# Kernel tuning notes

Measured on AMD Instinct MI355X. Metric: run time of the kernel, lower is better.

## Reference

```python
import jax, jax.numpy as jnp
import numpy as np

# Config constants derived from init_kwargs
VX, VY = 0.16, 0.16
X0, Y0 = 0.0, -39.68
X_OFF = VX / 2 + X0
Y_OFF = VY / 2 + Y0
X_L, Y_L = 432, 496  # round((x1-x0)/vx), round((y1-y0)/vy)
B = 4
C_OUT = 64
BN_EPS = 1e-3


def setup_inputs() -> dict:
    key = jax.random.key(0)
    ks = jax.random.split(key, 9)
    M, P = 64000, 32
    pillars = jax.random.normal(ks[0], (M, P, 4), dtype=jnp.float32)
    b_id = jax.random.randint(ks[1], (M,), 0, B, dtype=jnp.int32)
    z_id = jnp.zeros((M,), dtype=jnp.int32)
    y_id = jax.random.randint(ks[2], (M,), 0, Y_L, dtype=jnp.int32)
    x_id = jax.random.randint(ks[3], (M,), 0, X_L, dtype=jnp.int32)
    coors = jnp.stack([b_id, z_id, y_id, x_id], axis=1)
    nums = jax.random.randint(ks[4], (M,), 1, P + 1, dtype=jnp.int32)
    W = jax.random.normal(ks[5], (C_OUT, 9), dtype=jnp.float32) * 0.1
    gamma = 1.0 + 0.1 * jax.random.normal(ks[6], (C_OUT,), dtype=jnp.float32)
    beta = 0.1 * jax.random.normal(ks[7], (C_OUT,), dtype=jnp.float32)
    running_mean = 0.1 * jax.random.normal(ks[8], (C_OUT,), dtype=jnp.float32)
    running_var = jax.random.uniform(ks[8], (C_OUT,), dtype=jnp.float32, minval=0.5, maxval=1.5)
    return {"pillars": pillars, "coors": coors, "nums": nums, "W": W,
            "gamma": gamma, "beta": beta,
            "running_mean": running_mean, "running_var": running_var}


def reference(pillars, coors, nums, W, gamma, beta, running_mean, running_var):
    M, P, _ = pillars.shape
    numsf = nums.astype(jnp.float32)
    point_mask = (jnp.arange(P)[None, :] < nums[:, None]).astype(pillars.dtype)  # [M,P]

    # mean of valid xyz per pillar, center features
    masked_xyz = pillars[:, :, :3] * point_mask[:, :, None]
    mean = masked_xyz.sum(axis=1, keepdims=True) / jnp.clip(numsf, 1.0)[:, None, None]
    f_centered = pillars[:, :, :3] - mean

    # offsets from pillar center
    x_c = coors[:, 3].astype(jnp.float32) * VX + X_OFF
    y_c = coors[:, 2].astype(jnp.float32) * VY + Y_OFF
    f_x = pillars[:, :, 0:1] - x_c[:, None, None]
    f_y = pillars[:, :, 1:2] - y_c[:, None, None]

    features = jnp.concatenate([pillars, f_centered, f_x, f_y], axis=2)  # [M,P,9]
    features = features * point_mask[:, :, None]

    # 1x1 conv + eval-mode BN + ReLU, then max over points
    h = jnp.einsum('mpc,oc->mpo', features, W)  # [M,P,C_OUT]
    scale = gamma / jnp.sqrt(running_var + BN_EPS)
    h = jax.nn.relu(h * scale + (beta - running_mean * scale))
    pooled = h.max(axis=1)  # [M,C_OUT]

    b = coors[:, 0]
    y = coors[:, 2]
    x = coors[:, 3]
    valid = (x >= 0) & (x < X_L) & (y >= 0) & (y < Y_L)
    y_s = jnp.where(valid, y, Y_L)
    x_s = jnp.where(valid, x, X_L)
    canvas = jnp.zeros((B, Y_L, X_L, C_OUT), dtype=pooled.dtype)
    canvas = canvas.at[b, y_s, x_s].set(pooled, mode='drop')
    return canvas.transpose(0, 3, 1, 2)  # [B, C_OUT, Y_L, X_L]
```

## Files before the change

kernel.cpp:

```cpp
#include <hip/hip_runtime.h>

#define XL 432
#define XL4 108
#define YL 496
#define CELLS_B (YL * XL)
#define PLANE4 (CELLS_B / 4)
#define BN 4
#define COUT 64
#define PP 32
#define TCELLS 128
#define TG 32
#define LSTR 132

__global__ __launch_bounds__(256) void winner_kernel(const int* __restrict__ coors,
                                                     int* __restrict__ winner, int M) {
    int m = blockIdx.x * blockDim.x + threadIdx.x;
    if (m >= M) return;
    int b = coors[4 * m + 0];
    int y = coors[4 * m + 2];
    int x = coors[4 * m + 3];
    if (x < 0 || x >= XL || y < 0 || y >= YL) return;
    atomicMax(&winner[(b * YL + y) * XL + x], m);
}

__global__ __launch_bounds__(256) void pillar_compute(
    const float* __restrict__ pillars,
    const int* __restrict__ coors,
    const int* __restrict__ nums,
    const float* __restrict__ W,
    const float* __restrict__ gamma, const float* __restrict__ beta,
    const float* __restrict__ rmean, const float* __restrict__ rvar,
    float* __restrict__ pooled,
    int M) {
    const int pb   = threadIdx.x >> 6;
    const int lane = threadIdx.x & 63;
    const int m    = blockIdx.x * 4 + pb;

    __shared__ float4 pts[4][PP];

    if (m < M && lane < PP) {
        pts[pb][lane] = ((const float4*)pillars)[m * PP + lane];
    }
    __syncthreads();
    if (m >= M) return;

    const int x = coors[4 * m + 3];
    const int y = coors[4 * m + 2];

    int num = nums[m];
    if (num < 1) num = 1;
    if (num > PP) num = PP;

    const float scale = gamma[lane] * rsqrtf(rvar[lane] + 1e-3f);
    const float bias  = beta[lane] - rmean[lane] * scale;

    float sx = 0.f, sy = 0.f, sz = 0.f;
    for (int p = 0; p < num; ++p) {
        float4 q = pts[pb][p];
        sx += q.x; sy += q.y; sz += q.z;
    }
    const float inv = 1.0f / (float)num;
    const float mx = sx * inv, my = sy * inv, mz = sz * inv;

    const float xc = (float)x * 0.16f + 0.08f;
    const float yc = (float)y * 0.16f + (0.08f - 39.68f);

    const float w0 = W[lane * 9 + 0], w1 = W[lane * 9 + 1], w2 = W[lane * 9 + 2];
    const float w3 = W[lane * 9 + 3], w4 = W[lane * 9 + 4], w5 = W[lane * 9 + 5];
    const float w6 = W[lane * 9 + 6], w7 = W[lane * 9 + 7], w8 = W[lane * 9 + 8];

    float acc = (num < PP) ? fmaxf(bias, 0.0f) : 0.0f;

    for (int p = 0; p < num; ++p) {
        float4 q = pts[pb][p];
        float h = q.x * w0 + q.y * w1 + q.z * w2 + q.w * w3
                + (q.x - mx) * w4 + (q.y - my) * w5 + (q.z - mz) * w6
                + (q.x - xc) * w7 + (q.y - yc) * w8;
        float v = h * scale + bias;
        acc = fmaxf(acc, fmaxf(v, 0.0f));
    }

    pooled[m * COUT + lane] = acc;
}

__global__ __launch_bounds__(256) void canvas_kernel(
    const int* __restrict__ winner,
    const float* __restrict__ pooled,
    float4* __restrict__ out4) {
    __shared__ float lds[COUT * LSTR];

    const int t   = threadIdx.x;
    const int b   = blockIdx.y;
    const int blk = blockIdx.x;
    const int baseCell = blk * TCELLS;

    {
        const int cell = t >> 1;
        const int h    = t & 1;
        const int w = winner[b * CELLS_B + baseCell + cell];

        float4 r[8];
        if (w >= 0) {
            const float4* row = (const float4*)(pooled + (size_t)w * COUT) + h * 8;
            #pragma unroll
            for (int k = 0; k < 8; ++k) r[k] = row[k];
        } else {
            #pragma unroll
            for (int k = 0; k < 8; ++k) r[k] = make_float4(0.f, 0.f, 0.f, 0.f);
        }
        #pragma unroll
        for (int k = 0; k < 8; ++k) {
            const int cb = h * 32 + 4 * k;
            lds[(cb + 0) * LSTR + cell] = r[k].x;
            lds[(cb + 1) * LSTR + cell] = r[k].y;
            lds[(cb + 2) * LSTR + cell] = r[k].z;
            lds[(cb + 3) * LSTR + cell] = r[k].w;
        }
    }
    __syncthreads();

    {
        const int xg  = t & 31;
        const int chi = t >> 5;
        float4* outb = out4 + (size_t)b * COUT * PLANE4 + (size_t)blk * TG + xg;
        #pragma unroll
        for (int cc = 0; cc < 8; ++cc) {
            const int c = cc * 8 + chi;
            const float4 v = *(const float4*)&lds[c * LSTR + 4 * xg];
            outb[(size_t)c * PLANE4] = v;
        }
    }
}

extern "C" void kernel_launch(void* const* d_in, const int* in_sizes, int n_in,
                              void* d_out, int out_size, void* d_ws, size_t ws_size,
                              hipStream_t stream) {
    const float* pillars = (const float*)d_in[0];
    const int*   coors   = (const int*)d_in[1];
    const int*   nums    = (const int*)d_in[2];
    const float* W       = (const float*)d_in[3];
    const float* gamma   = (const float*)d_in[4];
    const float* beta    = (const float*)d_in[5];
    const float* rmean   = (const float*)d_in[6];
    const float* rvar    = (const float*)d_in[7];
    float* out = (float*)d_out;

    const int M = in_sizes[2];
    int*   winner = (int*)d_ws;
    float* pooled = (float*)((char*)d_ws + (size_t)BN * CELLS_B * sizeof(int));

    hipMemsetAsync(winner, 0xFF, (size_t)BN * CELLS_B * sizeof(int), stream);

    winner_kernel<<<(M + 255) / 256, 256, 0, stream>>>(coors, winner, M);
    pillar_compute<<<(M + 3) / 4, 256, 0, stream>>>(
        pillars, coors, nums, W, gamma, beta, rmean, rvar, pooled, M);

    dim3 cgrid(CELLS_B / TCELLS, BN);
    canvas_kernel<<<cgrid, 256, 0, stream>>>(winner, pooled, (float4*)out);
}
```

Before: 305.5 us.

## Collapse per-point conv via linearity, skip losing pillars, widen canvas blocks

The per-pillar conv is rewritten so that each output channel is an affine function of one projection per point. Only the max or min of that projection, picked by the sign of the BN scale, is needed, so the loop runs once. Pillars that lose the last-write-wins scatter now skip compute. Coordinate reads use int4 vector loads, and the canvas kernel moves to 512 threads with nontemporal stores. The risk is float rounding differences from the reassociated arithmetic, and losing pillars still pay for their point loads before the winner check.

```diff
diff --git a/kernel.cpp b/kernel.cpp
--- a/kernel.cpp
+++ b/kernel.cpp
@@ -1,7 +1,6 @@
 #include <hip/hip_runtime.h>
 
 #define XL 432
-#define XL4 108
 #define YL 496
 #define CELLS_B (YL * XL)
 #define PLANE4 (CELLS_B / 4)
@@ -12,15 +11,15 @@
 #define TG 32
 #define LSTR 132
 
+typedef float v4f __attribute__((ext_vector_type(4)));
+
 __global__ __launch_bounds__(256) void winner_kernel(const int* __restrict__ coors,
                                                      int* __restrict__ winner, int M) {
     int m = blockIdx.x * blockDim.x + threadIdx.x;
     if (m >= M) return;
-    int b = coors[4 * m + 0];
-    int y = coors[4 * m + 2];
-    int x = coors[4 * m + 3];
-    if (x < 0 || x >= XL || y < 0 || y >= YL) return;
-    atomicMax(&winner[(b * YL + y) * XL + x], m);
+    const int4 c = ((const int4*)coors)[m];
+    if (c.w < 0 || c.w >= XL || c.z < 0 || c.z >= YL) return;
+    atomicMax(&winner[(c.x * YL + c.z) * XL + c.w], m);
 }
 
 __global__ __launch_bounds__(256) void pillar_compute(
@@ -30,6 +29,7 @@
     const float* __restrict__ W,
     const float* __restrict__ gamma, const float* __restrict__ beta,
     const float* __restrict__ rmean, const float* __restrict__ rvar,
+    const int* __restrict__ winner,
     float* __restrict__ pooled,
     int M) {
     const int pb   = threadIdx.x >> 6;
@@ -44,8 +44,10 @@
     __syncthreads();
     if (m >= M) return;
 
-    const int x = coors[4 * m + 3];
-    const int y = coors[4 * m + 2];
+    const int4 co = ((const int4*)coors)[m];
+    const int x = co.w, y = co.z;
+    if (x < 0 || x >= XL || y < 0 || y >= YL) return;
+    if (winner[(co.x * YL + y) * XL + x] != m) return;
 
     int num = nums[m];
     if (num < 1) num = 1;
@@ -54,39 +56,36 @@
     const float scale = gamma[lane] * rsqrtf(rvar[lane] + 1e-3f);
     const float bias  = beta[lane] - rmean[lane] * scale;
 
-    float sx = 0.f, sy = 0.f, sz = 0.f;
-    for (int p = 0; p < num; ++p) {
-        float4 q = pts[pb][p];
-        sx += q.x; sy += q.y; sz += q.z;
-    }
-    const float inv = 1.0f / (float)num;
-    const float mx = sx * inv, my = sy * inv, mz = sz * inv;
-
-    const float xc = (float)x * 0.16f + 0.08f;
-    const float yc = (float)y * 0.16f + (0.08f - 39.68f);
-
     const float w0 = W[lane * 9 + 0], w1 = W[lane * 9 + 1], w2 = W[lane * 9 + 2];
     const float w3 = W[lane * 9 + 3], w4 = W[lane * 9 + 4], w5 = W[lane * 9 + 5];
     const float w6 = W[lane * 9 + 6], w7 = W[lane * 9 + 7], w8 = W[lane * 9 + 8];
+    const float cwx = w0 + w4 + w7, cwy = w1 + w5 + w8, cwz = w2 + w6, cww = w3;
 
-    float acc = (num < PP) ? fmaxf(bias, 0.0f) : 0.0f;
+    float sx = 0.f, sy = 0.f, sz = 0.f;
+    float dmax = -3.0e38f, dmin = 3.0e38f;
+    for (int p = 0; p < num; ++p) {
+        const float4 q = pts[pb][p];
+        sx += q.x; sy += q.y; sz += q.z;
+        const float d = q.x * cwx + q.y * cwy + q.z * cwz + q.w * cww;
+        dmax = fmaxf(dmax, d);
+        dmin = fminf(dmin, d);
+    }
+    const float inv = 1.0f / (float)num;
+    const float xc = (float)x * 0.16f + 0.08f;
+    const float yc = (float)y * 0.16f + (0.08f - 39.68f);
+    const float C0 = sx * inv * w4 + sy * inv * w5 + sz * inv * w6
+                   + xc * w7 + yc * w8;
 
-    for (int p = 0; p < num; ++p) {
-        float4 q = pts[pb][p];
-        float h = q.x * w0 + q.y * w1 + q.z * w2 + q.w * w3
-                + (q.x - mx) * w4 + (q.y - my) * w5 + (q.z - mz) * w6
-                + (q.x - xc) * w7 + (q.y - yc) * w8;
-        float v = h * scale + bias;
-        acc = fmaxf(acc, fmaxf(v, 0.0f));
-    }
-
-    pooled[m * COUT + lane] = acc;
+    const float sel = (scale >= 0.f) ? dmax : dmin;
+    float v = (sel - C0) * scale + bias;
+    if (num < PP) v = fmaxf(v, bias);
+    pooled[m * COUT + lane] = fmaxf(v, 0.f);
 }
 
-__global__ __launch_bounds__(256) void canvas_kernel(
+__global__ __launch_bounds__(512) void canvas_kernel(
     const int* __restrict__ winner,
     const float* __restrict__ pooled,
-    float4* __restrict__ out4) {
+    v4f* __restrict__ out4) {
     __shared__ float lds[COUT * LSTR];
 
     const int t   = threadIdx.x;
@@ -95,22 +94,22 @@
     const int baseCell = blk * TCELLS;
 
     {
-        const int cell = t >> 1;
-        const int h    = t & 1;
+        const int cell = t >> 2;
+        const int qq   = t & 3;
         const int w = winner[b * CELLS_B + baseCell + cell];
 
-        float4 r[8];
+        float4 r[4];
         if (w >= 0) {
-            const float4* row = (const float4*)(pooled + (size_t)w * COUT) + h * 8;
+            const float4* row = (const float4*)(pooled + (size_t)w * COUT);
             #pragma unroll
-            for (int k = 0; k < 8; ++k) r[k] = row[k];
+            for (int k = 0; k < 4; ++k) r[k] = row[qq + 4 * k];
         } else {
             #pragma unroll
-            for (int k = 0; k < 8; ++k) r[k] = make_float4(0.f, 0.f, 0.f, 0.f);
+            for (int k = 0; k < 4; ++k) r[k] = make_float4(0.f, 0.f, 0.f, 0.f);
         }
         #pragma unroll
-        for (int k = 0; k < 8; ++k) {
-            const int cb = h * 32 + 4 * k;
+        for (int k = 0; k < 4; ++k) {
+            const int cb = 4 * (qq + 4 * k);
             lds[(cb + 0) * LSTR + cell] = r[k].x;
             lds[(cb + 1) * LSTR + cell] = r[k].y;
             lds[(cb + 2) * LSTR + cell] = r[k].z;
@@ -122,12 +121,12 @@
     {
         const int xg  = t & 31;
         const int chi = t >> 5;
-        float4* outb = out4 + (size_t)b * COUT * PLANE4 + (size_t)blk * TG + xg;
+        v4f* outb = out4 + (size_t)b * COUT * PLANE4 + (size_t)blk * TG + xg;
         #pragma unroll
-        for (int cc = 0; cc < 8; ++cc) {
-            const int c = cc * 8 + chi;
-            const float4 v = *(const float4*)&lds[c * LSTR + 4 * xg];
-            outb[(size_t)c * PLANE4] = v;
+        for (int cc = 0; cc < 4; ++cc) {
+            const int c = cc * 16 + chi;
+            const v4f v = *(const v4f*)&lds[c * LSTR + 4 * xg];
+            __builtin_nontemporal_store(v, &outb[(size_t)c * PLANE4]);
         }
     }
 }
@@ -149,12 +148,12 @@
     int*   winner = (int*)d_ws;
     float* pooled = (float*)((char*)d_ws + (size_t)BN * CELLS_B * sizeof(int));
 
-    hipMemsetAsync(winner, 0xFF, (size_t)BN * CELLS_B * sizeof(int), stream);
+    (void)hipMemsetAsync(winner, 0xFF, (size_t)BN * CELLS_B * sizeof(int), stream);
 
     winner_kernel<<<(M + 255) / 256, 256, 0, stream>>>(coors, winner, M);
     pillar_compute<<<(M + 3) / 4, 256, 0, stream>>>(
-        pillars, coors, nums, W, gamma, beta, rmean, rvar, pooled, M);
+        pillars, coors, nums, W, gamma, beta, rmean, rvar, winner, pooled, M);
 
     dim3 cgrid(CELLS_B / TCELLS, BN);
-    canvas_kernel<<<cgrid, 256, 0, stream>>>(winner, pooled, (float4*)out);
+    canvas_kernel<<<cgrid, 512, 0, stream>>>(winner, pooled, (v4f*)out);
 }
```

Measured after the change: 298.9 us. 1.02x faster.
